# Performance work log

Measured on AMD Instinct MI355X. Metric: run time of the kernel, lower is better.

## Reference

```python
import jax, jax.numpy as jnp
import numpy as np

# --- model constants (match init_kwargs / Mamba2 defaults) ---
NUM_BLOCKS = 2
D_MODEL = 768
EXPAND = 2
D_INNER = EXPAND * D_MODEL          # 1536
D_STATE = 128
D_CONV = 4
HEADDIM = 64
NHEADS = D_INNER // HEADDIM         # 24
CONV_DIM = D_INNER + 2 * D_STATE    # 1792 (x, B, C go through the depthwise conv)
D_IN_PROJ = 2 * D_INNER + 2 * D_STATE + NHEADS  # 3352
VOCAB = 32000
LABEL_DIM = 1000
EPS = 1e-5


def _layernorm(x, w, b):
    mu = jnp.mean(x, axis=-1, keepdims=True)
    var = jnp.mean(jnp.square(x - mu), axis=-1, keepdims=True)
    return (x - mu) * jax.lax.rsqrt(var + EPS) * w + b


def _dwconv_causal(x, w, b):
    # x: [B, L, C], w: [C, K] depthwise kernel, b: [C]
    C, K = w.shape
    xt = jnp.transpose(x, (0, 2, 1))  # [B, C, L]
    out = jax.lax.conv_general_dilated(
        xt, w[:, None, :], window_strides=(1,), padding=[(K - 1, 0)],
        feature_group_count=C, dimension_numbers=("NCH", "OIH", "NCH"))
    return jnp.transpose(out, (0, 2, 1)) + b


def _ssd_scan(xh, Bm, Cm, dt, A):
    # xh: [B,L,H,P], Bm/Cm: [B,L,N], dt: [B,L,H], A: [H]
    Bsz, L, H, P = xh.shape
    N = Bm.shape[-1]
    dA = jnp.exp(dt * A)  # [B,L,H], in (0,1)

    def step(h, inp):
        xt, bt, ct, dat, dtt = inp  # [B,H,P],[B,N],[B,N],[B,H],[B,H]
        h = h * dat[:, :, None, None] + (dtt[:, :, None, None] * xt[..., None]) * bt[:, None, None, :]
        y = jnp.einsum('bhpn,bn->bhp', h, ct)
        return h, y

    h0 = jnp.zeros((Bsz, H, P, N), dtype=xh.dtype)
    xs = (jnp.transpose(xh, (1, 0, 2, 3)),
          jnp.transpose(Bm, (1, 0, 2)),
          jnp.transpose(Cm, (1, 0, 2)),
          jnp.transpose(dA, (1, 0, 2)),
          jnp.transpose(dt, (1, 0, 2)))
    _, ys = jax.lax.scan(step, h0, xs)  # ys: [L,B,H,P]
    return jnp.transpose(ys, (1, 0, 2, 3))


def _mamba2(x, Win, conv_w, conv_b, dt_bias, A_log, Dp, rms_w, Wout):
    Bsz, L, _ = x.shape
    zxbcdt = x @ Win  # [B,L,D_IN_PROJ]
    z = zxbcdt[..., :D_INNER]
    xBC = zxbcdt[..., D_INNER:D_INNER + CONV_DIM]
    dt = zxbcdt[..., D_INNER + CONV_DIM:]  # [B,L,H]
    dt = jax.nn.softplus(dt + dt_bias)

    xBC = jax.nn.silu(_dwconv_causal(xBC, conv_w, conv_b))
    xs = xBC[..., :D_INNER]
    Bm = xBC[..., D_INNER:D_INNER + D_STATE]
    Cm = xBC[..., D_INNER + D_STATE:]

    xh = xs.reshape(Bsz, L, NHEADS, HEADDIM)
    A = -jnp.exp(A_log)  # [H]
    y = _ssd_scan(xh, Bm, Cm, dt, A) + Dp[None, None, :, None] * xh  # [B,L,H,P]
    y = y.reshape(Bsz, L, D_INNER)

    # gated RMSNorm: norm(y * silu(z)) * weight
    y = y * jax.nn.silu(z)
    y = y * jax.lax.rsqrt(jnp.mean(jnp.square(y), axis=-1, keepdims=True) + EPS) * rms_w
    return y @ Wout


def _forward(tokens, emb, ln_w, ln_b, Win, conv_w, conv_b, dt_bias, A_log, Dp, rms_w, Wout, Wcls, bcls):
    x = emb[tokens]  # [B,L,D_MODEL]
    for i in range(NUM_BLOCKS):
        nx = _layernorm(x, ln_w[i], ln_b[i])
        x = x + _mamba2(nx, Win[i], conv_w[i], conv_b[i], dt_bias[i],
                        A_log[i], Dp[i], rms_w[i], Wout[i])
        # dropout_rate=0 (eval) -> identity; use_glu=False -> no post stage
    return x @ Wcls + bcls


def setup_inputs() -> dict:
    key = jax.random.key(0)
    ks = jax.random.split(key, 12)
    B, L = 2, 512
    tokens = jax.random.randint(ks[0], (B, L), 0, VOCAB)
    emb = jax.random.normal(ks[1], (VOCAB, D_MODEL), jnp.float32) * 0.02
    ln_w = jnp.ones((NUM_BLOCKS, D_MODEL), jnp.float32)
    ln_b = jnp.zeros((NUM_BLOCKS, D_MODEL), jnp.float32)
    Win = jax.random.normal(ks[2], (NUM_BLOCKS, D_MODEL, D_IN_PROJ), jnp.float32) / np.sqrt(D_MODEL)
    conv_w = jax.random.normal(ks[3], (NUM_BLOCKS, CONV_DIM, D_CONV), jnp.float32) / np.sqrt(D_CONV)
    conv_b = jnp.zeros((NUM_BLOCKS, CONV_DIM), jnp.float32)
    dt0 = jax.random.uniform(ks[4], (NUM_BLOCKS, NHEADS), jnp.float32, 1e-3, 0.1)
    dt_bias = dt0 + jnp.log(-jnp.expm1(-dt0))  # inverse softplus
    A_log = jnp.log(jax.random.uniform(ks[5], (NUM_BLOCKS, NHEADS), jnp.float32, 1.0, 16.0))
    Dp = jnp.ones((NUM_BLOCKS, NHEADS), jnp.float32)
    rms_w = jnp.ones((NUM_BLOCKS, D_INNER), jnp.float32)
    Wout = jax.random.normal(ks[6], (NUM_BLOCKS, D_INNER, D_MODEL), jnp.float32) / np.sqrt(D_INNER)
    Wcls = jax.random.normal(ks[7], (D_MODEL, LABEL_DIM), jnp.float32) / np.sqrt(D_MODEL)
    bcls = jnp.zeros((LABEL_DIM,), jnp.float32)
    return {"tokens": tokens, "emb": emb, "ln_w": ln_w, "ln_b": ln_b, "Win": Win,
            "conv_w": conv_w, "conv_b": conv_b, "dt_bias": dt_bias, "A_log": A_log,
            "Dp": Dp, "rms_w": rms_w, "Wout": Wout, "Wcls": Wcls, "bcls": bcls}


def reference(tokens, emb, ln_w, ln_b, Win, conv_w, conv_b, dt_bias, A_log, Dp, rms_w, Wout, Wcls, bcls):
    return _forward(tokens, emb, ln_w, ln_b, Win, conv_w, conv_b, dt_bias, A_log, Dp, rms_w, Wout, Wcls, bcls)
```

## Files before the change

kernel.cpp:

```cpp
#include <hip/hip_runtime.h>
#include <hip/hip_bf16.h>
#include <math.h>

#define B_SZ 2
#define L_SEQ 512
#define DMODEL 768
#define DINNER 1536
#define DSTATE 128
#define HEADDIM 64
#define NHEADS 24
#define CONVDIM 1792
#define DINPROJ 3352
#define ROWS (B_SZ * L_SEQ)

#define CHUNK 32
#define NCHUNK (L_SEQ / CHUNK)
#define BCDIM (2 * DSTATE)

#define NPAD_IN 3456
#define NPAD_CLS 1024

typedef __attribute__((ext_vector_type(8))) __bf16 bf16x8;
typedef __attribute__((ext_vector_type(4))) __bf16 bf16x4;
typedef __attribute__((ext_vector_type(4))) float f32x4;

typedef __attribute__((address_space(1))) const unsigned int as1_u32;
typedef __attribute__((address_space(3))) unsigned int as3_u32;

__device__ __forceinline__ void gload16(const void* g, void* s) {
  __builtin_amdgcn_global_load_lds((as1_u32*)(unsigned long)g, (as3_u32*)(unsigned long)s, 16, 0,
                                   0);
}

__device__ __forceinline__ float siluf(float x) { return x / (1.f + expf(-x)); }
__device__ __forceinline__ float softplusf(float x) {
  return x > 0.f ? x + log1pf(expf(-x)) : log1pf(expf(x));
}

__device__ __forceinline__ float block_reduce_sum(float v, float* sred) {
  int tid = threadIdx.x;
  for (int off = 32; off; off >>= 1) v += __shfl_down(v, off, 64);
  int wid = tid >> 6, lane = tid & 63;
  if (lane == 0) sred[wid] = v;
  __syncthreads();
  float total;
  if (tid == 0) {
    total = 0.f;
    int nw = blockDim.x >> 6;
    for (int i = 0; i < nw; ++i) total += sred[i];
    sred[0] = total;
  }
  __syncthreads();
  total = sred[0];
  __syncthreads();
  return total;
}

__global__ __launch_bounds__(256) void decomp_all_kernel(
    const float* __restrict__ Win, const float* __restrict__ Wout,
    const float* __restrict__ Wcls, const int* __restrict__ tok, const float* __restrict__ emb,
    const float* __restrict__ lnw0, const float* __restrict__ lnb0, float* __restrict__ x,
    __bf16* __restrict__ nxh, __bf16* __restrict__ nxl, __bf16* __restrict__ wih0,
    __bf16* __restrict__ wil0, __bf16* __restrict__ wih1, __bf16* __restrict__ wil1,
    __bf16* __restrict__ woh0, __bf16* __restrict__ wol0, __bf16* __restrict__ woh1,
    __bf16* __restrict__ wol1, __bf16* __restrict__ wch, __bf16* __restrict__ wcl) {
  constexpr int TIN = (NPAD_IN / 32) * (DMODEL / 32);
  constexpr int TOUT = (DMODEL / 32) * (DINNER / 32);
  constexpr int TCLS = (NPAD_CLS / 32) * (DMODEL / 32);
  __shared__ float tile[32][33];
  int bid = blockIdx.x;
  int tid = threadIdx.x;

  if (bid >= 2 * TIN + 2 * TOUT + TCLS) {
    int row = bid - (2 * TIN + 2 * TOUT + TCLS);
    int t = tok[row];
    float v[3];
    float s = 0.f;
#pragma unroll
    for (int j = 0; j < 3; ++j) {
      v[j] = emb[(size_t)t * DMODEL + tid + j * 256];
      s += v[j];
      x[(size_t)row * DMODEL + tid + j * 256] = v[j];
    }
    float* sred = (float*)tile;
    float mean = block_reduce_sum(s, sred) * (1.f / DMODEL);
    float s2 = 0.f;
#pragma unroll
    for (int j = 0; j < 3; ++j) {
      float d = v[j] - mean;
      s2 += d * d;
    }
    float var = block_reduce_sum(s2, sred) * (1.f / DMODEL);
    float r = 1.f / sqrtf(var + 1e-5f);
#pragma unroll
    for (int j = 0; j < 3; ++j) {
      int d = tid + j * 256;
      float val = (v[j] - mean) * r * lnw0[d] + lnb0[d];
      __bf16 h = (__bf16)val;
      nxh[(size_t)row * DMODEL + d] = h;
      nxl[(size_t)row * DMODEL + d] = (__bf16)(val - (float)h);
    }
    return;
  }

  const float* W;
  __bf16 *Th, *Tl;
  int K, N, ntx, r;
  if (bid < TIN) {
    W = Win; Th = wih0; Tl = wil0; K = DMODEL; N = DINPROJ; ntx = NPAD_IN / 32; r = bid;
  } else if (bid < 2 * TIN) {
    W = Win + (size_t)DMODEL * DINPROJ; Th = wih1; Tl = wil1; K = DMODEL; N = DINPROJ;
    ntx = NPAD_IN / 32; r = bid - TIN;
  } else if (bid < 2 * TIN + TOUT) {
    W = Wout; Th = woh0; Tl = wol0; K = DINNER; N = DMODEL; ntx = DMODEL / 32; r = bid - 2 * TIN;
  } else if (bid < 2 * TIN + 2 * TOUT) {
    W = Wout + (size_t)DINNER * DMODEL; Th = woh1; Tl = wol1; K = DINNER; N = DMODEL;
    ntx = DMODEL / 32; r = bid - 2 * TIN - TOUT;
  } else {
    W = Wcls; Th = wch; Tl = wcl; K = DMODEL; N = 1000; ntx = NPAD_CLS / 32;
    r = bid - 2 * TIN - 2 * TOUT;
  }
  int bn = (r % ntx) * 32, bk = (r / ntx) * 32;

  int i = tid >> 3, j4 = (tid & 7) * 4;
  int kk = bk + i;
  int nn = bn + j4;
  float4 v;
  if (nn + 3 < N) {
    v = *(const float4*)(W + (size_t)kk * N + nn);
  } else {
    v.x = (nn + 0 < N) ? W[(size_t)kk * N + nn + 0] : 0.f;
    v.y = (nn + 1 < N) ? W[(size_t)kk * N + nn + 1] : 0.f;
    v.z = (nn + 2 < N) ? W[(size_t)kk * N + nn + 2] : 0.f;
    v.w = (nn + 3 < N) ? W[(size_t)kk * N + nn + 3] : 0.f;
  }
  tile[i][j4 + 0] = v.x;
  tile[i][j4 + 1] = v.y;
  tile[i][j4 + 2] = v.z;
  tile[i][j4 + 3] = v.w;
  __syncthreads();
  int n = bn + i;
  bf16x4 hv, lv;
#pragma unroll
  for (int q = 0; q < 4; ++q) {
    float f = tile[j4 + q][i];
    __bf16 h = (__bf16)f;
    hv[q] = h;
    lv[q] = (__bf16)(f - (float)h);
  }
  *(bf16x4*)(Th + (size_t)n * K + bk + j4) = hv;
  *(bf16x4*)(Tl + (size_t)n * K + bk + j4) = lv;
}

__global__ __launch_bounds__(256) void ln_kernel(const float* __restrict__ x,
                                                 const float* __restrict__ w,
                                                 const float* __restrict__ b,
                                                 __bf16* __restrict__ oh,
                                                 __bf16* __restrict__ ol) {
  __shared__ float sred[8];
  int row = blockIdx.x, tid = threadIdx.x;
  const float* xr = x + (size_t)row * DMODEL;
  float v[3];
  float s = 0.f;
#pragma unroll
  for (int j = 0; j < 3; ++j) {
    v[j] = xr[tid + j * 256];
    s += v[j];
  }
  float mean = block_reduce_sum(s, sred) * (1.f / DMODEL);
  float s2 = 0.f;
#pragma unroll
  for (int j = 0; j < 3; ++j) {
    float d = v[j] - mean;
    s2 += d * d;
  }
  float var = block_reduce_sum(s2, sred) * (1.f / DMODEL);
  float r = 1.f / sqrtf(var + 1e-5f);
#pragma unroll
  for (int j = 0; j < 3; ++j) {
    int d = tid + j * 256;
    float val = (v[j] - mean) * r * w[d] + b[d];
    __bf16 h = (__bf16)val;
    oh[(size_t)row * DMODEL + d] = h;
    ol[(size_t)row * DMODEL + d] = (__bf16)(val - (float)h);
  }
}

__global__ __launch_bounds__(256) void act_decomp_kernel(const float* __restrict__ x,
                                                         __bf16* __restrict__ oh,
                                                         __bf16* __restrict__ ol) {
  int row = blockIdx.x, tid = threadIdx.x;
#pragma unroll
  for (int j = 0; j < 3; ++j) {
    int d = tid + j * 256;
    float v = x[(size_t)row * DMODEL + d];
    __bf16 h = (__bf16)v;
    oh[(size_t)row * DMODEL + d] = h;
    ol[(size_t)row * DMODEL + d] = (__bf16)(v - (float)h);
  }
}

template <int FM, int FN, bool ATOMIC>
__global__ __launch_bounds__(256) void mfma_gemm_kernel(
    const __bf16* __restrict__ Ahi, const __bf16* __restrict__ Alo,
    const __bf16* __restrict__ Bhi, const __bf16* __restrict__ Blo,
    const float* __restrict__ addsrc, const float* __restrict__ bias, float* __restrict__ C,
    int N, int K, int kslice) {
  constexpr int BM = FM * 32;
  constexpr int BN = FN * 32;
  constexpr int RGA = BM / 16;
  constexpr int RGB = BN / 16;
  constexpr int NITER = (2 * (RGA + RGB)) / 4;
  constexpr int ABYTES = BM * 64;
  constexpr int BBYTES = BN * 64;
  constexpr int BUFBYTES = 2 * ABYTES + 2 * BBYTES;
  __shared__ char lds[2 * BUFBYTES];

  int tid = threadIdx.x;
  int wave = tid >> 6, lane = tid & 63;
  int wm = wave >> 1, wn = wave & 1;
  int bm = blockIdx.y * BM;
  int bn = blockIdx.x * BN;
  int kbeg = ATOMIC ? blockIdx.z * kslice : 0;
  int kend = ATOMIC ? (kbeg + kslice) : K;
  int l2 = lane >> 2;
  int gch = (lane & 3) ^ ((lane >> 3) & 3);
  int lr = lane & 15, lg = lane >> 4;

  f32x4 acc[FM][FN] = {};

  auto stage = [&](char* buf, int k0) {
#pragma unroll
    for (int it = 0; it < NITER; ++it) {
      int rg = wave + it * 4;
      const __bf16* src;
      int row0, boff;
      if (rg < RGA) {
        src = Ahi;
        row0 = bm + rg * 16;
        boff = rg * 1024;
      } else if (rg < 2 * RGA) {
        src = Alo;
        row0 = bm + (rg - RGA) * 16;
        boff = ABYTES + (rg - RGA) * 1024;
      } else if (rg < 2 * RGA + RGB) {
        src = Bhi;
        row0 = bn + (rg - 2 * RGA) * 16;
        boff = 2 * ABYTES + (rg - 2 * RGA) * 1024;
      } else {
        src = Blo;
        row0 = bn + (rg - 2 * RGA - RGB) * 16;
        boff = 2 * ABYTES + BBYTES + (rg - 2 * RGA - RGB) * 1024;
      }
      gload16(src + (size_t)(row0 + l2) * K + k0 + gch * 8, buf + boff);
    }
  };

  stage(lds, kbeg);
  __syncthreads();

  char* curb = lds;
  char* nxtb = lds + BUFBYTES;
  for (int k0 = kbeg; k0 < kend; k0 += 32) {
    if (k0 + 32 < kend) stage(nxtb, k0 + 32);

    bf16x8 ahi[FM], alo[FM], bhi[FN], blo[FN];
#pragma unroll
    for (int m = 0; m < FM; ++m) {
      int r = wm * FM * 16 + m * 16 + lr;
      int off = r * 64 + ((lg ^ ((r >> 1) & 3)) * 16);
      ahi[m] = *(const bf16x8*)(curb + off);
      alo[m] = *(const bf16x8*)(curb + ABYTES + off);
    }
#pragma unroll
    for (int n = 0; n < FN; ++n) {
      int r = wn * FN * 16 + n * 16 + lr;
      int off = r * 64 + ((lg ^ ((r >> 1) & 3)) * 16);
      bhi[n] = *(const bf16x8*)(curb + 2 * ABYTES + off);
      blo[n] = *(const bf16x8*)(curb + 2 * ABYTES + BBYTES + off);
    }
#pragma unroll
    for (int m = 0; m < FM; ++m)
#pragma unroll
      for (int n = 0; n < FN; ++n) {
        acc[m][n] = __builtin_amdgcn_mfma_f32_16x16x32_bf16(ahi[m], bhi[n], acc[m][n], 0, 0, 0);
        acc[m][n] = __builtin_amdgcn_mfma_f32_16x16x32_bf16(ahi[m], blo[n], acc[m][n], 0, 0, 0);
        acc[m][n] = __builtin_amdgcn_mfma_f32_16x16x32_bf16(alo[m], bhi[n], acc[m][n], 0, 0, 0);
      }
    __syncthreads();
    char* t = curb;
    curb = nxtb;
    nxtb = t;
  }

#pragma unroll
  for (int m = 0; m < FM; ++m) {
#pragma unroll
    for (int n = 0; n < FN; ++n) {
      int gcol = bn + wn * FN * 16 + n * 16 + lr;
      if (gcol < N) {
#pragma unroll
        for (int r = 0; r < 4; ++r) {
          int grow = bm + wm * FM * 16 + m * 16 + lg * 4 + r;
          if (ATOMIC) {
            unsafeAtomicAdd(&C[(size_t)grow * N + gcol], acc[m][n][r]);
          } else {
            float v = acc[m][n][r];
            if (addsrc) v += addsrc[(size_t)grow * N + gcol];
            if (bias) v += bias[gcol];
            C[(size_t)grow * N + gcol] = v;
          }
        }
      }
    }
  }
}

__global__ __launch_bounds__(256) void convBC_kernel(const float* __restrict__ zx,
                                                     const float* __restrict__ cw,
                                                     const float* __restrict__ cb,
                                                     const float* __restrict__ dtb,
                                                     float* __restrict__ xBC,
                                                     float* __restrict__ dts) {
  int row = blockIdx.x;
  int c = threadIdx.x;
  int ch = DINNER + c;
  int l = row & (L_SEQ - 1);
  float acc = cb[ch];
#pragma unroll
  for (int k = 0; k < 4; ++k) {
    int ls = l - 3 + k;
    if (ls >= 0)
      acc = fmaf(cw[ch * 4 + k], zx[(size_t)(row - 3 + k) * DINPROJ + DINNER + ch], acc);
  }
  xBC[(size_t)row * BCDIM + c] = siluf(acc);
  if (c < NHEADS) {
    float raw = zx[(size_t)row * DINPROJ + DINNER + CONVDIM + c] + dtb[c];
    dts[(size_t)row * NHEADS + c] = softplusf(raw);
  }
}

__global__ __launch_bounds__(256) void sraw_kernel(const float* __restrict__ xBC,
                                                   float* __restrict__ Sraw) {
  __shared__ float Bs[CHUNK][132];
  __shared__ float Cs[CHUNK][132];
  int ci = blockIdx.x, b = blockIdx.y;
  int tid = threadIdx.x;
  int row0 = b * L_SEQ + ci * CHUNK;
#pragma unroll
  for (int i = 0; i < 4; ++i) {
    int vi = tid + i * 256;
    int t = vi >> 5;
    int n4 = (vi & 31) * 4;
    const float* r = xBC + (size_t)(row0 + t) * BCDIM;
    *(float4*)&Bs[t][n4] = *(const float4*)(r + n4);
    *(float4*)&Cs[t][n4] = *(const float4*)(r + DSTATE + n4);
  }
  __syncthreads();
  int t0 = (tid >> 4) * 2;
  int s0 = (tid & 15) * 2;
  float sacc[2][2] = {};
#pragma unroll
  for (int n = 0; n < DSTATE; n += 4) {
    float cr[2][4], br[2][4];
#pragma unroll
    for (int i = 0; i < 2; ++i) *(float4*)&cr[i][0] = *(const float4*)&Cs[t0 + i][n];
#pragma unroll
    for (int j = 0; j < 2; ++j) *(float4*)&br[j][0] = *(const float4*)&Bs[s0 + j][n];
#pragma unroll
    for (int i = 0; i < 2; ++i)
#pragma unroll
      for (int j = 0; j < 2; ++j)
#pragma unroll
        for (int k = 0; k < 4; ++k) sacc[i][j] = fmaf(cr[i][k], br[j][k], sacc[i][j]);
  }
  float* Sp = Sraw + ((size_t)(b * NCHUNK + ci) * CHUNK) * CHUNK;
#pragma unroll
  for (int i = 0; i < 2; ++i)
#pragma unroll
    for (int j = 0; j < 2; ++j) Sp[(t0 + i) * CHUNK + s0 + j] = sacc[i][j];
}

__global__ __launch_bounds__(256) void chunk_local_kernel(
    const float* __restrict__ zx, const float* __restrict__ xBC, const float* __restrict__ Sraw,
    const float* __restrict__ dts, const float* __restrict__ cw, const float* __restrict__ cb,
    const float* __restrict__ Alog, const float* __restrict__ Dp, float* __restrict__ y,
    float* __restrict__ G, float* __restrict__ et, float* __restrict__ elast) {
  __shared__ float Bs[CHUNK][132];
  __shared__ float Xs[CHUNK][68];
  __shared__ float Ss[CHUNK][36];
  __shared__ float sP[CHUNK], sW[CHUNK], sDt[CHUNK];

  int ci = blockIdx.x, h = blockIdx.y, b = blockIdx.z;
  int bh = b * NHEADS + h;
  int tid = threadIdx.x;
  int row0 = b * L_SEQ + ci * CHUNK;

#pragma unroll
  for (int i = 0; i < 2; ++i) {
    int vi = tid + i * 256;
    int t = vi >> 4;
    int n8 = (vi & 15) * 8;
    const float* r = xBC + (size_t)(row0 + t) * BCDIM;
    *(float4*)&Bs[t][n8] = *(const float4*)(r + n8);
    *(float4*)&Bs[t][n8 + 4] = *(const float4*)(r + n8 + 4);
  }
#pragma unroll
  for (int i = 0; i < 2; ++i) {
    int vi = tid + i * 256;
    int t = vi >> 4;
    int p4 = (vi & 15) * 4;
    int cX = h * HEADDIM + p4;
    float oX[4];
#pragma unroll
    for (int q = 0; q < 4; ++q) oX[q] = cb[cX + q];
#pragma unroll
    for (int k = 0; k < 4; ++k) {
      if (ci > 0 || t + k >= 3) {
        float4 v = *(const float4*)(zx + (size_t)(row0 + t - 3 + k) * DINPROJ + DINNER + cX);
#pragma unroll
        for (int q = 0; q < 4; ++q) oX[q] = fmaf(cw[(cX + q) * 4 + k], ((const float*)&v)[q], oX[q]);
      }
    }
#pragma unroll
    for (int q = 0; q < 4; ++q) Xs[t][p4 + q] = siluf(oX[q]);
  }
  if (tid < 32) {
    int t = tid;
    float Ah = -expf(Alog[h]);
    float dtv = dts[(size_t)(row0 + t) * NHEADS + h];
    float P = dtv * Ah;
#pragma unroll
    for (int off = 1; off < 32; off <<= 1) {
      float u = __shfl_up(P, off, 32);
      if (t >= off) P += u;
    }
    float Plast = __shfl(P, 31, 32);
    float e = expf(P);
    sP[t] = P;
    sDt[t] = dtv;
    sW[t] = expf(Plast - P) * dtv;
    et[(size_t)(bh * NCHUNK + ci) * CHUNK + t] = e;
    if (t == 31) elast[bh * NCHUNK + ci] = e;
  }
  __syncthreads();

  int t0 = (tid >> 4) * 2;
  int s0 = (tid & 15) * 2;
  {
    const float* Sp = Sraw + ((size_t)(b * NCHUNK + ci) * CHUNK) * CHUNK;
#pragma unroll
    for (int i = 0; i < 2; ++i)
#pragma unroll
      for (int j = 0; j < 2; ++j) {
        int t = t0 + i, s = s0 + j;
        float sr = Sp[t * CHUNK + s];
        Ss[t][s] = (t >= s) ? sr * expf(sP[t] - sP[s]) * sDt[s] : 0.f;
      }
  }
  __syncthreads();

  {
    int p0 = (tid & 15) * 4;
    float acc[2][4] = {};
#pragma unroll
    for (int s = 0; s < CHUNK; s += 4) {
      float sr[2][4], xr[4][4];
#pragma unroll
      for (int i = 0; i < 2; ++i) *(float4*)&sr[i][0] = *(const float4*)&Ss[t0 + i][s];
#pragma unroll
      for (int u = 0; u < 4; ++u) *(float4*)&xr[u][0] = *(const float4*)&Xs[s + u][p0];
#pragma unroll
      for (int i = 0; i < 2; ++i)
#pragma unroll
        for (int j = 0; j < 4; ++j)
#pragma unroll
          for (int u = 0; u < 4; ++u) acc[i][j] = fmaf(sr[i][u], xr[u][j], acc[i][j]);
    }
    float Dh = Dp[h];
#pragma unroll
    for (int i = 0; i < 2; ++i) {
      int row = row0 + t0 + i;
      float4 o;
      o.x = acc[i][0] + Dh * Xs[t0 + i][p0 + 0];
      o.y = acc[i][1] + Dh * Xs[t0 + i][p0 + 1];
      o.z = acc[i][2] + Dh * Xs[t0 + i][p0 + 2];
      o.w = acc[i][3] + Dh * Xs[t0 + i][p0 + 3];
      *(float4*)(y + (size_t)row * DINNER + h * HEADDIM + p0) = o;
    }
  }

  {
    int n0 = (tid >> 4) * 8;
    int p0 = (tid & 15) * 4;
    float g[8][4] = {};
#pragma unroll 4
    for (int s = 0; s < CHUNK; ++s) {
      float w = sW[s];
      float bv[8], xv[4];
      *(float4*)&bv[0] = *(const float4*)&Bs[s][n0];
      *(float4*)&bv[4] = *(const float4*)&Bs[s][n0 + 4];
      *(float4*)&xv[0] = *(const float4*)&Xs[s][p0];
#pragma unroll
      for (int k = 0; k < 8; ++k) {
        float wb = w * bv[k];
#pragma unroll
        for (int j = 0; j < 4; ++j) g[k][j] = fmaf(wb, xv[j], g[k][j]);
      }
    }
    float* Gp = G + ((size_t)bh * NCHUNK + ci) * (DSTATE * HEADDIM);
#pragma unroll
    for (int k = 0; k < 8; ++k) {
      *(float4*)(Gp + (size_t)(n0 + k) * HEADDIM + p0) = *(float4*)&g[k][0];
    }
  }
}

__global__ __launch_bounds__(256) void combine_kernel(float* __restrict__ G,
                                                      const float* __restrict__ elast) {
  int part = blockIdx.x;
  int bh = blockIdx.y;
  int gi = part * 256 + threadIdx.x;
  float4* base = (float4*)(G + (size_t)bh * NCHUNK * (DSTATE * HEADDIM));
  const float* el = elast + bh * NCHUNK;
  float4 h = {0.f, 0.f, 0.f, 0.f};
#pragma unroll
  for (int c = 0; c < NCHUNK - 1; ++c) {
    float4 g = base[(size_t)c * 2048 + gi];
    float e = el[c];
    h.x = fmaf(e, h.x, g.x);
    h.y = fmaf(e, h.y, g.y);
    h.z = fmaf(e, h.z, g.z);
    h.w = fmaf(e, h.w, g.w);
    base[(size_t)c * 2048 + gi] = h;
  }
}

__global__ __launch_bounds__(256) void apply_inter_kernel(const float* __restrict__ xBC,
                                                          const float* __restrict__ G,
                                                          const float* __restrict__ et,
                                                          float* __restrict__ y) {
  __shared__ float Cs[CHUNK][132];
  __shared__ float Hs[DSTATE][68];
  __shared__ float sE[CHUNK];
  int ci = blockIdx.x + 1;
  int h = blockIdx.y, b = blockIdx.z;
  int bh = b * NHEADS + h;
  int tid = threadIdx.x;
  int row0 = b * L_SEQ + ci * CHUNK;

#pragma unroll
  for (int i = 0; i < 4; ++i) {
    int vi = tid + i * 256;
    int t = vi >> 5;
    int n4 = (vi & 31) * 4;
    *(float4*)&Cs[t][n4] = *(const float4*)(xBC + (size_t)(row0 + t) * BCDIM + DSTATE + n4);
  }
  const float* Hsrc = G + ((size_t)bh * NCHUNK + (ci - 1)) * (DSTATE * HEADDIM);
#pragma unroll
  for (int i = 0; i < 8; ++i) {
    int vi = tid + i * 256;
    int n = vi >> 4;
    int p4 = (vi & 15) * 4;
    *(float4*)&Hs[n][p4] = *(const float4*)(Hsrc + (size_t)n * HEADDIM + p4);
  }
  if (tid < CHUNK) sE[tid] = et[(size_t)(bh * NCHUNK + ci) * CHUNK + tid];
  __syncthreads();

  int t0 = (tid >> 4) * 2;
  int p0 = (tid & 15) * 4;
  float acc[2][4] = {};
#pragma unroll
  for (int n = 0; n < DSTATE; n += 4) {
    float cr[2][4], hr[4][4];
#pragma unroll
    for (int i = 0; i < 2; ++i) *(float4*)&cr[i][0] = *(const float4*)&Cs[t0 + i][n];
#pragma unroll
    for (int u = 0; u < 4; ++u) *(float4*)&hr[u][0] = *(const float4*)&Hs[n + u][p0];
#pragma unroll
    for (int i = 0; i < 2; ++i)
#pragma unroll
      for (int j = 0; j < 4; ++j)
#pragma unroll
        for (int u = 0; u < 4; ++u) acc[i][j] = fmaf(cr[i][u], hr[u][j], acc[i][j]);
  }
#pragma unroll
  for (int i = 0; i < 2; ++i) {
    int row = row0 + t0 + i;
    float e = sE[t0 + i];
    float* yp = y + (size_t)row * DINNER + h * HEADDIM + p0;
    float4 cur = *(float4*)yp;
    cur.x = fmaf(e, acc[i][0], cur.x);
    cur.y = fmaf(e, acc[i][1], cur.y);
    cur.z = fmaf(e, acc[i][2], cur.z);
    cur.w = fmaf(e, acc[i][3], cur.w);
    *(float4*)yp = cur;
  }
}

__global__ __launch_bounds__(256) void gate_rms_kernel(const float* __restrict__ y,
                                                       const float* __restrict__ zx,
                                                       const float* __restrict__ rmsw,
                                                       __bf16* __restrict__ oh,
                                                       __bf16* __restrict__ ol) {
  __shared__ float sred[8];
  int row = blockIdx.x, tid = threadIdx.x;
  const float* z = zx + (size_t)row * DINPROJ;
  const float* yr = y + (size_t)row * DINNER;
  float v[6];
  float ss = 0.f;
#pragma unroll
  for (int j = 0; j < 6; ++j) {
    int d = tid + j * 256;
    float val = yr[d] * siluf(z[d]);
    v[j] = val;
    ss += val * val;
  }
  float total = block_reduce_sum(ss, sred);
  float r = 1.f / sqrtf(total * (1.f / DINNER) + 1e-5f);
#pragma unroll
  for (int j = 0; j < 6; ++j) {
    int d = tid + j * 256;
    float val = v[j] * r * rmsw[d];
    __bf16 h = (__bf16)val;
    oh[(size_t)row * DINNER + d] = h;
    ol[(size_t)row * DINNER + d] = (__bf16)(val - (float)h);
  }
}

extern "C" void kernel_launch(void* const* d_in, const int* in_sizes, int n_in,
                              void* d_out, int out_size, void* d_ws, size_t ws_size,
                              hipStream_t stream) {
  const int* tokens = (const int*)d_in[0];
  const float* emb = (const float*)d_in[1];
  const float* ln_w = (const float*)d_in[2];
  const float* ln_b = (const float*)d_in[3];
  const float* Win = (const float*)d_in[4];
  const float* conv_w = (const float*)d_in[5];
  const float* conv_b = (const float*)d_in[6];
  const float* dt_bias = (const float*)d_in[7];
  const float* A_log = (const float*)d_in[8];
  const float* Dp = (const float*)d_in[9];
  const float* rms_w = (const float*)d_in[10];
  const float* Wout = (const float*)d_in[11];
  const float* Wcls = (const float*)d_in[12];
  const float* bcls = (const float*)d_in[13];
  float* out = (float*)d_out;

  float* ws = (float*)d_ws;
  float* x = ws;
  float* zx = x + (size_t)ROWS * DMODEL;
  float* y = zx + (size_t)ROWS * DINPROJ;
  float* G = y + (size_t)ROWS * DINNER;
  float* et = G + (size_t)B_SZ * NHEADS * NCHUNK * DSTATE * HEADDIM;
  float* elast = et + (size_t)B_SZ * NHEADS * NCHUNK * CHUNK;
  float* xBC = elast + B_SZ * NHEADS * NCHUNK;
  float* Sraw = xBC + (size_t)ROWS * BCDIM;
  float* dts = Sraw + (size_t)B_SZ * NCHUNK * CHUNK * CHUNK;
  __bf16* bp = (__bf16*)(dts + (size_t)ROWS * NHEADS);
  __bf16* nxh = bp;  bp += (size_t)ROWS * DMODEL;
  __bf16* nxl = bp;  bp += (size_t)ROWS * DMODEL;
  __bf16* yh = bp;   bp += (size_t)ROWS * DINNER;
  __bf16* yl = bp;   bp += (size_t)ROWS * DINNER;
  __bf16* xh = bp;   bp += (size_t)ROWS * DMODEL;
  __bf16* xl = bp;   bp += (size_t)ROWS * DMODEL;
  __bf16* wih0 = bp; bp += (size_t)NPAD_IN * DMODEL;
  __bf16* wil0 = bp; bp += (size_t)NPAD_IN * DMODEL;
  __bf16* wih1 = bp; bp += (size_t)NPAD_IN * DMODEL;
  __bf16* wil1 = bp; bp += (size_t)NPAD_IN * DMODEL;
  __bf16* woh0 = bp; bp += (size_t)DMODEL * DINNER;
  __bf16* wol0 = bp; bp += (size_t)DMODEL * DINNER;
  __bf16* woh1 = bp; bp += (size_t)DMODEL * DINNER;
  __bf16* wol1 = bp; bp += (size_t)DMODEL * DINNER;
  __bf16* wch = bp;  bp += (size_t)NPAD_CLS * DMODEL;
  __bf16* wcl = bp;

  constexpr int TIN = (NPAD_IN / 32) * (DMODEL / 32);
  constexpr int TOUT = (DMODEL / 32) * (DINNER / 32);
  constexpr int TCLS = (NPAD_CLS / 32) * (DMODEL / 32);
  decomp_all_kernel<<<2 * TIN + 2 * TOUT + TCLS + ROWS, 256, 0, stream>>>(
      Win, Wout, Wcls, tokens, emb, ln_w, ln_b, x, nxh, nxl, wih0, wil0, wih1, wil1, woh0, wol0,
      woh1, wol1, wch, wcl);

  for (int blk = 0; blk < 2; ++blk) {
    const float* cw_b = conv_w + (size_t)blk * CONVDIM * 4;
    const float* cb_b = conv_b + (size_t)blk * CONVDIM;
    const float* dtb_b = dt_bias + (size_t)blk * NHEADS;
    const float* Alog_b = A_log + (size_t)blk * NHEADS;
    const float* Dp_b = Dp + (size_t)blk * NHEADS;
    const float* rmsw_b = rms_w + (size_t)blk * DINNER;
    __bf16* wih = blk ? wih1 : wih0;
    __bf16* wil = blk ? wil1 : wil0;
    __bf16* woh = blk ? woh1 : woh0;
    __bf16* wol = blk ? wol1 : wol0;

    if (blk == 1) {
      ln_kernel<<<ROWS, 256, 0, stream>>>(x, ln_w + (size_t)blk * DMODEL,
                                          ln_b + (size_t)blk * DMODEL, nxh, nxl);
    }

    mfma_gemm_kernel<2, 2, false><<<dim3(NPAD_IN / 64, ROWS / 64), 256, 0, stream>>>(
        nxh, nxl, wih, wil, nullptr, nullptr, zx, DINPROJ, DMODEL, 0);

    convBC_kernel<<<ROWS, BCDIM, 0, stream>>>(zx, cw_b, cb_b, dtb_b, xBC, dts);

    sraw_kernel<<<dim3(NCHUNK, B_SZ), 256, 0, stream>>>(xBC, Sraw);

    chunk_local_kernel<<<dim3(NCHUNK, NHEADS, B_SZ), 256, 0, stream>>>(
        zx, xBC, Sraw, dts, cw_b, cb_b, Alog_b, Dp_b, y, G, et, elast);

    combine_kernel<<<dim3(8, B_SZ * NHEADS), 256, 0, stream>>>(G, elast);

    apply_inter_kernel<<<dim3(NCHUNK - 1, NHEADS, B_SZ), 256, 0, stream>>>(xBC, G, et, y);

    gate_rms_kernel<<<ROWS, 256, 0, stream>>>(y, zx, rmsw_b, yh, yl);

    mfma_gemm_kernel<2, 2, true><<<dim3(DMODEL / 64, ROWS / 64, 4), 256, 0, stream>>>(
        yh, yl, woh, wol, nullptr, nullptr, x, DMODEL, DINNER, DINNER / 4);
  }

  act_decomp_kernel<<<ROWS, 256, 0, stream>>>(x, xh, xl);
  mfma_gemm_kernel<2, 2, false><<<dim3(NPAD_CLS / 64, ROWS / 64), 256, 0, stream>>>(
      xh, xl, wch, wcl, nullptr, bcls, out, 1000, DMODEL, 0);
}
```

Before: 255.6 us.

## Store chunk states in bf16 and remap GEMM workgroups across XCDs

The per-chunk state buffer G moves from fp32 to bf16. The chunk_local, combine and apply_inter kernels now write and read half the bytes, and the combine recurrence still accumulates in fp32 registers. The in-projection and classifier GEMMs now launch on a 1D grid, and block indices are remapped so consecutive tiles land on the same XCD, which is meant to improve L2 reuse. Rounding the states to bf16 loses precision in the scan and may hurt accuracy tolerance.

```diff
diff --git a/kernel.cpp b/kernel.cpp
--- a/kernel.cpp
+++ b/kernel.cpp
@@ -205,7 +205,7 @@
     const __bf16* __restrict__ Ahi, const __bf16* __restrict__ Alo,
     const __bf16* __restrict__ Bhi, const __bf16* __restrict__ Blo,
     const float* __restrict__ addsrc, const float* __restrict__ bias, float* __restrict__ C,
-    int N, int K, int kslice) {
+    int N, int K, int kslice, int nbx, int nwg) {
   constexpr int BM = FM * 32;
   constexpr int BN = FN * 32;
   constexpr int RGA = BM / 16;
@@ -219,8 +219,17 @@
   int tid = threadIdx.x;
   int wave = tid >> 6, lane = tid & 63;
   int wm = wave >> 1, wn = wave & 1;
-  int bm = blockIdx.y * BM;
-  int bn = blockIdx.x * BN;
+  int bx, by;
+  if (nbx > 0) {
+    int orig = (blockIdx.x % 8) * (nwg / 8) + blockIdx.x / 8;
+    bx = orig % nbx;
+    by = orig / nbx;
+  } else {
+    bx = blockIdx.x;
+    by = blockIdx.y;
+  }
+  int bm = by * BM;
+  int bn = bx * BN;
   int kbeg = ATOMIC ? blockIdx.z * kslice : 0;
   int kend = ATOMIC ? (kbeg + kslice) : K;
   int l2 = lane >> 2;
@@ -385,7 +394,7 @@
     const float* __restrict__ zx, const float* __restrict__ xBC, const float* __restrict__ Sraw,
     const float* __restrict__ dts, const float* __restrict__ cw, const float* __restrict__ cb,
     const float* __restrict__ Alog, const float* __restrict__ Dp, float* __restrict__ y,
-    float* __restrict__ G, float* __restrict__ et, float* __restrict__ elast) {
+    __bf16* __restrict__ G, float* __restrict__ et, float* __restrict__ elast) {
   __shared__ float Bs[CHUNK][132];
   __shared__ float Xs[CHUNK][68];
   __shared__ float Ss[CHUNK][36];
@@ -508,36 +517,44 @@
         for (int j = 0; j < 4; ++j) g[k][j] = fmaf(wb, xv[j], g[k][j]);
       }
     }
-    float* Gp = G + ((size_t)bh * NCHUNK + ci) * (DSTATE * HEADDIM);
+    __bf16* Gp = G + ((size_t)bh * NCHUNK + ci) * (DSTATE * HEADDIM);
 #pragma unroll
     for (int k = 0; k < 8; ++k) {
-      *(float4*)(Gp + (size_t)(n0 + k) * HEADDIM + p0) = *(float4*)&g[k][0];
-    }
-  }
-}
-
-__global__ __launch_bounds__(256) void combine_kernel(float* __restrict__ G,
+      bf16x4 o;
+#pragma unroll
+      for (int q = 0; q < 4; ++q) o[q] = (__bf16)g[k][q];
+      *(bf16x4*)(Gp + (size_t)(n0 + k) * HEADDIM + p0) = o;
+    }
+  }
+}
+
+__global__ __launch_bounds__(256) void combine_kernel(__bf16* __restrict__ G,
                                                       const float* __restrict__ elast) {
   int part = blockIdx.x;
   int bh = blockIdx.y;
   int gi = part * 256 + threadIdx.x;
-  float4* base = (float4*)(G + (size_t)bh * NCHUNK * (DSTATE * HEADDIM));
+  __bf16* base = G + (size_t)bh * NCHUNK * (DSTATE * HEADDIM);
   const float* el = elast + bh * NCHUNK;
-  float4 h = {0.f, 0.f, 0.f, 0.f};
+  float h0 = 0.f, h1 = 0.f, h2 = 0.f, h3 = 0.f;
 #pragma unroll
   for (int c = 0; c < NCHUNK - 1; ++c) {
-    float4 g = base[(size_t)c * 2048 + gi];
+    bf16x4 g = *(bf16x4*)(base + (size_t)c * (DSTATE * HEADDIM) + gi * 4);
     float e = el[c];
-    h.x = fmaf(e, h.x, g.x);
-    h.y = fmaf(e, h.y, g.y);
-    h.z = fmaf(e, h.z, g.z);
-    h.w = fmaf(e, h.w, g.w);
-    base[(size_t)c * 2048 + gi] = h;
+    h0 = fmaf(e, h0, (float)g[0]);
+    h1 = fmaf(e, h1, (float)g[1]);
+    h2 = fmaf(e, h2, (float)g[2]);
+    h3 = fmaf(e, h3, (float)g[3]);
+    bf16x4 o;
+    o[0] = (__bf16)h0;
+    o[1] = (__bf16)h1;
+    o[2] = (__bf16)h2;
+    o[3] = (__bf16)h3;
+    *(bf16x4*)(base + (size_t)c * (DSTATE * HEADDIM) + gi * 4) = o;
   }
 }
 
 __global__ __launch_bounds__(256) void apply_inter_kernel(const float* __restrict__ xBC,
-                                                          const float* __restrict__ G,
+                                                          const __bf16* __restrict__ G,
                                                           const float* __restrict__ et,
                                                           float* __restrict__ y) {
   __shared__ float Cs[CHUNK][132];
@@ -556,13 +573,15 @@
     int n4 = (vi & 31) * 4;
     *(float4*)&Cs[t][n4] = *(const float4*)(xBC + (size_t)(row0 + t) * BCDIM + DSTATE + n4);
   }
-  const float* Hsrc = G + ((size_t)bh * NCHUNK + (ci - 1)) * (DSTATE * HEADDIM);
+  const __bf16* Hsrc = G + ((size_t)bh * NCHUNK + (ci - 1)) * (DSTATE * HEADDIM);
 #pragma unroll
   for (int i = 0; i < 8; ++i) {
     int vi = tid + i * 256;
     int n = vi >> 4;
     int p4 = (vi & 15) * 4;
-    *(float4*)&Hs[n][p4] = *(const float4*)(Hsrc + (size_t)n * HEADDIM + p4);
+    bf16x4 g = *(const bf16x4*)(Hsrc + (size_t)n * HEADDIM + p4);
+#pragma unroll
+    for (int q = 0; q < 4; ++q) Hs[n][p4 + q] = (float)g[q];
   }
   if (tid < CHUNK) sE[tid] = et[(size_t)(bh * NCHUNK + ci) * CHUNK + tid];
   __syncthreads();
@@ -651,8 +670,8 @@
   float* x = ws;
   float* zx = x + (size_t)ROWS * DMODEL;
   float* y = zx + (size_t)ROWS * DINPROJ;
-  float* G = y + (size_t)ROWS * DINNER;
-  float* et = G + (size_t)B_SZ * NHEADS * NCHUNK * DSTATE * HEADDIM;
+  __bf16* G = (__bf16*)(y + (size_t)ROWS * DINNER);
+  float* et = (float*)(G + (size_t)B_SZ * NHEADS * NCHUNK * DSTATE * HEADDIM);
   float* elast = et + (size_t)B_SZ * NHEADS * NCHUNK * CHUNK;
   float* xBC = elast + B_SZ * NHEADS * NCHUNK;
   float* Sraw = xBC + (size_t)ROWS * BCDIM;
@@ -699,8 +718,9 @@
                                           ln_b + (size_t)blk * DMODEL, nxh, nxl);
     }
 
-    mfma_gemm_kernel<2, 2, false><<<dim3(NPAD_IN / 64, ROWS / 64), 256, 0, stream>>>(
-        nxh, nxl, wih, wil, nullptr, nullptr, zx, DINPROJ, DMODEL, 0);
+    mfma_gemm_kernel<2, 2, false><<<(NPAD_IN / 64) * (ROWS / 64), 256, 0, stream>>>(
+        nxh, nxl, wih, wil, nullptr, nullptr, zx, DINPROJ, DMODEL, 0, NPAD_IN / 64,
+        (NPAD_IN / 64) * (ROWS / 64));
 
     convBC_kernel<<<ROWS, BCDIM, 0, stream>>>(zx, cw_b, cb_b, dtb_b, xBC, dts);
 
@@ -716,10 +736,11 @@
     gate_rms_kernel<<<ROWS, 256, 0, stream>>>(y, zx, rmsw_b, yh, yl);
 
     mfma_gemm_kernel<2, 2, true><<<dim3(DMODEL / 64, ROWS / 64, 4), 256, 0, stream>>>(
-        yh, yl, woh, wol, nullptr, nullptr, x, DMODEL, DINNER, DINNER / 4);
+        yh, yl, woh, wol, nullptr, nullptr, x, DMODEL, DINNER, DINNER / 4, 0, 0);
   }
 
   act_decomp_kernel<<<ROWS, 256, 0, stream>>>(x, xh, xl);
-  mfma_gemm_kernel<2, 2, false><<<dim3(NPAD_CLS / 64, ROWS / 64), 256, 0, stream>>>(
-      xh, xl, wch, wcl, nullptr, bcls, out, 1000, DMODEL, 0);
-}
+  mfma_gemm_kernel<2, 2, false><<<(NPAD_CLS / 64) * (ROWS / 64), 256, 0, stream>>>(
+      xh, xl, wch, wcl, nullptr, bcls, out, 1000, DMODEL, 0, NPAD_CLS / 64,
+      (NPAD_CLS / 64) * (ROWS / 64));
+}
```

After: 249.2 us. -2.5%, faster.
